# Performance work log

Hardware: AMD Instinct MI355X
Metric: run time of the kernel (lower is better)

## Reference

```python
import jax, jax.numpy as jnp
import numpy as np

K = 7          # kernel_size
PAD = 3        # padding
GROUPS = 8
OUTC = 128
INC = 128
REFINE = True


def conv1x1(x, w):
    # x: [B,C,H,W], w: [O,C] (1x1 conv, no bias)
    return jnp.einsum('oc,bchw->bohw', w, x)


def unfold2d(x, k):
    # x: [B,C,Hp,Wp] -> [B,C,h,w,k,k], stride 1 (matches torch unfold(2,k).unfold(3,k))
    B, C, Hp, Wp = x.shape
    h, w = Hp - k + 1, Wp - k + 1
    patches = jnp.stack([x[:, :, i:i + h, j:j + w] for i in range(k) for j in range(k)], axis=-1)
    return patches.reshape(B, C, h, w, k, k)


def unfold1d(x, k, axis):
    # sliding window of size k, stride 1, along axis 2 (rows) or 3 (cols)
    if axis == 2:
        h = x.shape[2] - k + 1
        return jnp.stack([x[:, :, i:i + h, :] for i in range(k)], axis=-1)  # [B,C,h,W,k]
    else:
        w = x.shape[3] - k + 1
        return jnp.stack([x[:, :, :, j:j + w] for j in range(k)], axis=-1)  # [B,C,H,w,k]


def _forward(feature_map, wq, wk, wv, rel_h, rel_w):
    c = feature_map.shape[1] // 2
    fm_t0, fm_t1 = feature_map[:, :c], feature_map[:, c:]
    B, _, H, W = fm_t0.shape
    cg = OUTC // GROUPS

    padded_t0 = jnp.pad(fm_t0, ((0, 0), (0, 0), (PAD, PAD), (PAD, PAD)))
    q = conv1x1(fm_t1, wq)                 # [B,OUTC,H,W]
    k_full = conv1x1(padded_t0, wk)        # [B,OUTC,H+2p,W+2p]
    v_full = conv1x1(padded_t0, wv)

    k_win = unfold2d(k_full, K)            # [B,OUTC,H,W,K,K]
    k_h, k_w = k_win[:, :OUTC // 2], k_win[:, OUTC // 2:]
    k_win = jnp.concatenate([k_h + rel_h, k_w + rel_w], axis=1)
    k_win = k_win.reshape(B, GROUPS, cg, H, W, K * K)
    v_win = unfold2d(v_full, K).reshape(B, GROUPS, cg, H, W, K * K)

    qg = q.reshape(B, GROUPS, cg, H, W, 1)
    attn = jax.nn.softmax(jnp.sum(qg * k_win, axis=2), axis=-1)  # [B,G,H,W,K*K]
    out = jnp.einsum('bnhwk,bnchwk->bnchw', attn, v_win).reshape(B, OUTC, H, W)

    if REFINE:
        win = 2 * K + 1
        p_col = jnp.pad(fm_t0, ((0, 0), (0, 0), (K, K), (0, 0)))
        p_row = jnp.pad(fm_t0, ((0, 0), (0, 0), (0, 0), (K, K)))
        k_col = unfold1d(conv1x1(p_col, wk), win, 2).reshape(B, GROUPS, cg, H, W, win)
        k_row = unfold1d(conv1x1(p_row, wk), win, 3).reshape(B, GROUPS, cg, H, W, win)
        v_col = unfold1d(conv1x1(p_col, wv), win, 2).reshape(B, GROUPS, cg, H, W, win)
        v_row = unfold1d(conv1x1(p_row, wv), win, 3).reshape(B, GROUPS, cg, H, W, win)

        a_row = jax.nn.softmax(jnp.sum(qg * k_row, axis=2), axis=-1)
        a_col = jax.nn.softmax(jnp.sum(qg * k_col, axis=2), axis=-1)
        out = out + jnp.einsum('bnhwk,bnchwk->bnchw', a_row, v_row).reshape(B, OUTC, H, W)
        out = out + jnp.einsum('bnhwk,bnchwk->bnchw', a_col, v_col).reshape(B, OUTC, H, W)
    return out


def setup_inputs() -> dict:
    key = jax.random.key(0)
    ks = jax.random.split(key, 6)
    B, H, W = 2, 64, 64
    feature_map = jax.random.normal(ks[0], (B, 2 * INC, H, W), dtype=jnp.float32)
    # kaiming_normal fan_out for 1x1 conv: std = sqrt(2 / outc)
    std = float(np.sqrt(2.0 / OUTC))
    wq = jax.random.normal(ks[1], (OUTC, INC), dtype=jnp.float32) * std
    wk = jax.random.normal(ks[2], (OUTC, INC), dtype=jnp.float32) * std
    wv = jax.random.normal(ks[3], (OUTC, INC), dtype=jnp.float32) * std
    rel_h = jax.random.normal(ks[4], (OUTC // 2, 1, 1, K, 1), dtype=jnp.float32)
    rel_w = jax.random.normal(ks[5], (OUTC // 2, 1, 1, 1, K), dtype=jnp.float32)
    return {"feature_map": feature_map, "wq": wq, "wk": wk, "wv": wv,
            "rel_h": rel_h, "rel_w": rel_w}


def reference(feature_map, wq, wk, wv, rel_h, rel_w):
    return _forward(feature_map, wq, wk, wv, rel_h, rel_w)
```

## Files before the change

kernel.cpp:

```cpp
#include <hip/hip_runtime.h>
#include <hip/hip_bf16.h>

__device__ __forceinline__ float bf2f(unsigned short u) {
    union { unsigned int i; float f; } v; v.i = ((unsigned int)u) << 16; return v.f;
}
__device__ __forceinline__ unsigned short f2bf(float f) {
    __hip_bfloat16 h = __float2bfloat16(f);
    return *reinterpret_cast<unsigned short*>(&h);
}


__global__ __launch_bounds__(256) void conv_kernel(
    const float* __restrict__ fm,
    const float* __restrict__ wq, const float* __restrict__ wk,
    const float* __restrict__ wv,
    float* __restrict__ Qout,
    unsigned short* __restrict__ K0,
    unsigned short* __restrict__ V0)
{
    const int sel = blockIdx.y;
    const float* W = (sel == 0) ? wq : ((sel == 1) ? wk : wv);
    const int c0 = (sel == 0) ? 128 : 0;

    __shared__ float w_s[64 * 132];
    __shared__ float x_s[64 * 68];

    const int tid = threadIdx.x;
    const int P0  = blockIdx.x * 64;
    const int b   = P0 >> 12;
    const int hw0 = P0 & 4095;

    float acc[8][4];
    #pragma unroll
    for (int i = 0; i < 8; ++i)
        #pragma unroll
        for (int j = 0; j < 4; ++j) acc[i][j] = 0.f;

    const int ocb = (tid >> 4) * 8;
    const int pxb = (tid & 15) * 4;

    for (int kh = 0; kh < 128; kh += 64) {
        {
            const int o    = tid >> 1;
            const int koff = (tid & 1) * 32;
            #pragma unroll
            for (int i = 0; i < 8; ++i) {
                float4 v = *(const float4*)(W + o * 128 + kh + koff + i * 4);
                w_s[(koff + i * 4 + 0) * 132 + o] = v.x;
                w_s[(koff + i * 4 + 1) * 132 + o] = v.y;
                w_s[(koff + i * 4 + 2) * 132 + o] = v.z;
                w_s[(koff + i * 4 + 3) * 132 + o] = v.w;
            }
        }
        {
            const int c  = tid >> 2;
            const int pc = (tid & 3) * 16;
            const float* src = fm + (((size_t)(b * 256 + c0 + kh + c)) << 12) + hw0 + pc;
            #pragma unroll
            for (int i = 0; i < 4; ++i)
                *(float4*)(&x_s[c * 68 + pc + i * 4]) = *(const float4*)(src + i * 4);
        }
        __syncthreads();
        #pragma unroll 8
        for (int k = 0; k < 64; ++k) {
            const float* kw = &w_s[k * 132 + ocb];
            float4 wa = *(const float4*)kw;
            float4 wb = *(const float4*)(kw + 4);
            float4 xv = *(const float4*)(&x_s[k * 68 + pxb]);
            const float wf[8] = {wa.x, wa.y, wa.z, wa.w, wb.x, wb.y, wb.z, wb.w};
            const float xf[4] = {xv.x, xv.y, xv.z, xv.w};
            #pragma unroll
            for (int i = 0; i < 8; ++i)
                #pragma unroll
                for (int j = 0; j < 4; ++j) acc[i][j] += wf[i] * xf[j];
        }
        __syncthreads();
    }

    const int g   = ocb >> 4;
    const int lci = ocb & 8;
    #pragma unroll
    for (int pj = 0; pj < 4; ++pj) {
        const int hw = hw0 + pxb + pj;
        const size_t base = ((((size_t)(b * 8 + g)) << 12) + hw) * 16 + lci;
        if (sel == 0) {
            *(float4*)(Qout + base)     = make_float4(acc[0][pj], acc[1][pj], acc[2][pj], acc[3][pj]);
            *(float4*)(Qout + base + 4) = make_float4(acc[4][pj], acc[5][pj], acc[6][pj], acc[7][pj]);
        } else {
            unsigned short tmp[8];
            #pragma unroll
            for (int i = 0; i < 8; ++i) tmp[i] = f2bf(acc[i][pj]);
            unsigned short* dst = ((sel == 1) ? K0 : V0) + base;
            *(uint4*)dst = *(const uint4*)tmp;
        }
    }
}

struct KV16 { uint4 a, b; };
__device__ __forceinline__ KV16 ld16(const unsigned short* p) {
    KV16 r; r.a = *(const uint4*)p; r.b = *(const uint4*)(p + 8); return r;
}
__device__ __forceinline__ float dotq(const float* q, const KV16& k) {
    const unsigned short* u = (const unsigned short*)&k;
    float s = 0.f;
    #pragma unroll
    for (int c = 0; c < 16; ++c) s += q[c] * bf2f(u[c]);
    return s;
}
__device__ __forceinline__ void axpyq(float* acc, float wgt, const KV16& v) {
    const unsigned short* u = (const unsigned short*)&v;
    #pragma unroll
    for (int c = 0; c < 16; ++c) acc[c] += wgt * bf2f(u[c]);
}

__global__ __launch_bounds__(256) void attn_kernel(
    const float* __restrict__ Q,
    const unsigned short* __restrict__ K0,
    const unsigned short* __restrict__ V0,
    const float* __restrict__ rel_h,
    const float* __restrict__ rel_w,
    float* __restrict__ out)
{
    const int tid  = threadIdx.x;
    const int w    = tid & 63;
    const int h    = blockIdx.x * 4 + (tid >> 6);
    const int g    = blockIdx.y;
    const int b    = blockIdx.z / 3;
    const int part = blockIdx.z % 3;

    const size_t slab = ((size_t)(b * 8 + g)) << 16;
    const float* qptr = Q + slab + (size_t)(h * 64 + w) * 16;

    float qr[16];
    #pragma unroll
    for (int ci = 0; ci < 16; ++ci) qr[ci] = qptr[ci];

    const unsigned short* Kp = K0 + slab;
    const unsigned short* Vp = V0 + slab;

    float acc[16];
    #pragma unroll
    for (int ci = 0; ci < 16; ++ci) acc[ci] = 0.f;

    if (part == 0) {
        float qrel[7];
        const float* rel = (g < 4) ? (rel_h + g * 112) : (rel_w + (g - 4) * 112);
        #pragma unroll
        for (int t = 0; t < 7; ++t) {
            float s = 0.f;
            #pragma unroll
            for (int ci = 0; ci < 16; ++ci) s += qr[ci] * rel[ci * 7 + t];
            qrel[t] = s;
        }
        float sc[49];
        float mx = -3.4e38f;
        #pragma unroll
        for (int i = 0; i < 7; ++i) {
            const int y = h + i - 3;
            #pragma unroll
            for (int j = 0; j < 7; ++j) {
                const int x = w + j - 3;
                float d = 0.f;
                if (y >= 0 && y < 64 && x >= 0 && x < 64)
                    d = dotq(qr, ld16(Kp + (size_t)(y * 64 + x) * 16));
                d += qrel[(g < 4) ? i : j];
                sc[i * 7 + j] = d;
                mx = fmaxf(mx, d);
            }
        }
        float den = 0.f;
        #pragma unroll
        for (int k = 0; k < 49; ++k) { sc[k] = __expf(sc[k] - mx); den += sc[k]; }
        const float inv = 1.f / den;
        #pragma unroll
        for (int i = 0; i < 7; ++i) {
            const int y = h + i - 3;
            #pragma unroll
            for (int j = 0; j < 7; ++j) {
                const int x = w + j - 3;
                if (y >= 0 && y < 64 && x >= 0 && x < 64)
                    axpyq(acc, sc[i * 7 + j] * inv, ld16(Vp + (size_t)(y * 64 + x) * 16));
            }
        }
    } else if (part == 1) {
        float sc[15];
        float mx = -3.4e38f;
        #pragma unroll
        for (int j = 0; j < 15; ++j) {
            const int x = w + j - 7;
            float d = 0.f;
            if (x >= 0 && x < 64)
                d = dotq(qr, ld16(Kp + (size_t)(h * 64 + x) * 16));
            sc[j] = d; mx = fmaxf(mx, d);
        }
        float den = 0.f;
        #pragma unroll
        for (int j = 0; j < 15; ++j) { sc[j] = __expf(sc[j] - mx); den += sc[j]; }
        const float inv = 1.f / den;
        #pragma unroll
        for (int j = 0; j < 15; ++j) {
            const int x = w + j - 7;
            if (x >= 0 && x < 64)
                axpyq(acc, sc[j] * inv, ld16(Vp + (size_t)(h * 64 + x) * 16));
        }
    } else {
        float sc[15];
        float mx = -3.4e38f;
        #pragma unroll
        for (int i = 0; i < 15; ++i) {
            const int y = h + i - 7;
            float d = 0.f;
            if (y >= 0 && y < 64)
                d = dotq(qr, ld16(Kp + (size_t)(y * 64 + w) * 16));
            sc[i] = d; mx = fmaxf(mx, d);
        }
        float den = 0.f;
        #pragma unroll
        for (int i = 0; i < 15; ++i) { sc[i] = __expf(sc[i] - mx); den += sc[i]; }
        const float inv = 1.f / den;
        #pragma unroll
        for (int i = 0; i < 15; ++i) {
            const int y = h + i - 7;
            if (y >= 0 && y < 64)
                axpyq(acc, sc[i] * inv, ld16(Vp + (size_t)(y * 64 + w) * 16));
        }
    }

    float* op = out + (((size_t)(b * 128 + g * 16)) << 12) + h * 64 + w;
    #pragma unroll
    for (int ci = 0; ci < 16; ++ci)
        atomicAdd(op + ((size_t)ci << 12), acc[ci]);
}

extern "C" void kernel_launch(void* const* d_in, const int* in_sizes, int n_in,
                              void* d_out, int out_size, void* d_ws, size_t ws_size,
                              hipStream_t stream) {
    (void)in_sizes; (void)n_in; (void)ws_size;
    const float* fm    = (const float*)d_in[0];
    const float* wq    = (const float*)d_in[1];
    const float* wk    = (const float*)d_in[2];
    const float* wv    = (const float*)d_in[3];
    const float* rel_h = (const float*)d_in[4];
    const float* rel_w = (const float*)d_in[5];

    float* Q = (float*)d_ws;
    unsigned short* K0 = (unsigned short*)(Q + 1048576);
    unsigned short* V0 = K0 + 1048576;

    hipMemsetAsync(d_out, 0, (size_t)out_size * sizeof(float), stream);
    conv_kernel<<<dim3(128, 3, 1), dim3(256), 0, stream>>>(
        fm, wq, wk, wv, Q, K0, V0);
    attn_kernel<<<dim3(16, 8, 6), dim3(256), 0, stream>>>(
        Q, K0, V0, rel_h, rel_w, (float*)d_out);
}
```

Measured before the change: 115.3 us.

## Split each pixel's 16 channels across four lanes with quad shuffle reductions

The attention kernel now gives each output pixel four threads, each owning four channels. Dot products are finished with xor-shuffle reductions across the quad, and the grid grows fourfold, with one block covering one image row. Key/value loads for a window row are also batched into registers before use. The aim is to cut per-thread register pressure (sc[49] plus 16-wide accumulators) and raise occupancy and memory parallelism. The cost is extra shuffles and redundant softmax work done by all four lanes.

```diff
diff --git a/kernel.cpp b/kernel.cpp
--- a/kernel.cpp
+++ b/kernel.cpp
@@ -96,21 +96,14 @@
     }
 }
 
-struct KV16 { uint4 a, b; };
-__device__ __forceinline__ KV16 ld16(const unsigned short* p) {
-    KV16 r; r.a = *(const uint4*)p; r.b = *(const uint4*)(p + 8); return r;
-}
-__device__ __forceinline__ float dotq(const float* q, const KV16& k) {
+__device__ __forceinline__ float quadsum(float v) {
+    v += __shfl_xor(v, 1);
+    v += __shfl_xor(v, 2);
+    return v;
+}
+__device__ __forceinline__ float dot4(const float4& q, uint2 k) {
     const unsigned short* u = (const unsigned short*)&k;
-    float s = 0.f;
-    #pragma unroll
-    for (int c = 0; c < 16; ++c) s += q[c] * bf2f(u[c]);
-    return s;
-}
-__device__ __forceinline__ void axpyq(float* acc, float wgt, const KV16& v) {
-    const unsigned short* u = (const unsigned short*)&v;
-    #pragma unroll
-    for (int c = 0; c < 16; ++c) acc[c] += wgt * bf2f(u[c]);
+    return q.x * bf2f(u[0]) + q.y * bf2f(u[1]) + q.z * bf2f(u[2]) + q.w * bf2f(u[3]);
 }
 
 __global__ __launch_bounds__(256) void attn_kernel(
@@ -122,48 +115,46 @@
     float* __restrict__ out)
 {
     const int tid  = threadIdx.x;
-    const int w    = tid & 63;
-    const int h    = blockIdx.x * 4 + (tid >> 6);
+    const int s    = tid & 3;
+    const int w    = tid >> 2;
+    const int h    = blockIdx.x;
     const int g    = blockIdx.y;
     const int b    = blockIdx.z / 3;
     const int part = blockIdx.z % 3;
 
     const size_t slab = ((size_t)(b * 8 + g)) << 16;
-    const float* qptr = Q + slab + (size_t)(h * 64 + w) * 16;
-
-    float qr[16];
-    #pragma unroll
-    for (int ci = 0; ci < 16; ++ci) qr[ci] = qptr[ci];
-
-    const unsigned short* Kp = K0 + slab;
-    const unsigned short* Vp = V0 + slab;
-
-    float acc[16];
-    #pragma unroll
-    for (int ci = 0; ci < 16; ++ci) acc[ci] = 0.f;
+    const float4 qv = *(const float4*)(Q + slab + (size_t)(h * 64 + w) * 16 + s * 4);
+    const unsigned short* Kb = K0 + slab + s * 4;
+    const unsigned short* Vb = V0 + slab + s * 4;
+
+    float a0 = 0.f, a1 = 0.f, a2 = 0.f, a3 = 0.f;
+    const uint2 z2 = make_uint2(0u, 0u);
 
     if (part == 0) {
         float qrel[7];
-        const float* rel = (g < 4) ? (rel_h + g * 112) : (rel_w + (g - 4) * 112);
+        const float* rel = (g < 4) ? (rel_h + (g * 16 + s * 4) * 7)
+                                   : (rel_w + ((g - 4) * 16 + s * 4) * 7);
         #pragma unroll
         for (int t = 0; t < 7; ++t) {
-            float s = 0.f;
-            #pragma unroll
-            for (int ci = 0; ci < 16; ++ci) s += qr[ci] * rel[ci * 7 + t];
-            qrel[t] = s;
+            float pq = qv.x * rel[t] + qv.y * rel[7 + t]
+                     + qv.z * rel[14 + t] + qv.w * rel[21 + t];
+            qrel[t] = quadsum(pq);
         }
         float sc[49];
         float mx = -3.4e38f;
         #pragma unroll
         for (int i = 0; i < 7; ++i) {
             const int y = h + i - 3;
+            uint2 kr[7];
             #pragma unroll
             for (int j = 0; j < 7; ++j) {
                 const int x = w + j - 3;
-                float d = 0.f;
-                if (y >= 0 && y < 64 && x >= 0 && x < 64)
-                    d = dotq(qr, ld16(Kp + (size_t)(y * 64 + x) * 16));
-                d += qrel[(g < 4) ? i : j];
+                kr[j] = (y >= 0 && y < 64 && x >= 0 && x < 64)
+                      ? *(const uint2*)(Kb + (size_t)(y * 64 + x) * 16) : z2;
+            }
+            #pragma unroll
+            for (int j = 0; j < 7; ++j) {
+                float d = quadsum(dot4(qv, kr[j])) + qrel[(g < 4) ? i : j];
                 sc[i * 7 + j] = d;
                 mx = fmaxf(mx, d);
             }
@@ -175,22 +166,33 @@
         #pragma unroll
         for (int i = 0; i < 7; ++i) {
             const int y = h + i - 3;
+            uint2 vr[7];
             #pragma unroll
             for (int j = 0; j < 7; ++j) {
                 const int x = w + j - 3;
-                if (y >= 0 && y < 64 && x >= 0 && x < 64)
-                    axpyq(acc, sc[i * 7 + j] * inv, ld16(Vp + (size_t)(y * 64 + x) * 16));
+                vr[j] = (y >= 0 && y < 64 && x >= 0 && x < 64)
+                      ? *(const uint2*)(Vb + (size_t)(y * 64 + x) * 16) : z2;
+            }
+            #pragma unroll
+            for (int j = 0; j < 7; ++j) {
+                const float pw = sc[i * 7 + j] * inv;
+                const unsigned short* u = (const unsigned short*)&vr[j];
+                a0 += pw * bf2f(u[0]); a1 += pw * bf2f(u[1]);
+                a2 += pw * bf2f(u[2]); a3 += pw * bf2f(u[3]);
             }
         }
     } else if (part == 1) {
         float sc[15];
         float mx = -3.4e38f;
+        uint2 kr[15];
         #pragma unroll
         for (int j = 0; j < 15; ++j) {
             const int x = w + j - 7;
-            float d = 0.f;
-            if (x >= 0 && x < 64)
-                d = dotq(qr, ld16(Kp + (size_t)(h * 64 + x) * 16));
+            kr[j] = (x >= 0 && x < 64) ? *(const uint2*)(Kb + (size_t)(h * 64 + x) * 16) : z2;
+        }
+        #pragma unroll
+        for (int j = 0; j < 15; ++j) {
+            float d = quadsum(dot4(qv, kr[j]));
             sc[j] = d; mx = fmaxf(mx, d);
         }
         float den = 0.f;
@@ -200,18 +202,24 @@
         #pragma unroll
         for (int j = 0; j < 15; ++j) {
             const int x = w + j - 7;
-            if (x >= 0 && x < 64)
-                axpyq(acc, sc[j] * inv, ld16(Vp + (size_t)(h * 64 + x) * 16));
+            uint2 vv = (x >= 0 && x < 64) ? *(const uint2*)(Vb + (size_t)(h * 64 + x) * 16) : z2;
+            const float pw = sc[j] * inv;
+            const unsigned short* u = (const unsigned short*)&vv;
+            a0 += pw * bf2f(u[0]); a1 += pw * bf2f(u[1]);
+            a2 += pw * bf2f(u[2]); a3 += pw * bf2f(u[3]);
         }
     } else {
         float sc[15];
         float mx = -3.4e38f;
+        uint2 kr[15];
         #pragma unroll
         for (int i = 0; i < 15; ++i) {
             const int y = h + i - 7;
-            float d = 0.f;
-            if (y >= 0 && y < 64)
-                d = dotq(qr, ld16(Kp + (size_t)(y * 64 + w) * 16));
+            kr[i] = (y >= 0 && y < 64) ? *(const uint2*)(Kb + (size_t)(y * 64 + w) * 16) : z2;
+        }
+        #pragma unroll
+        for (int i = 0; i < 15; ++i) {
+            float d = quadsum(dot4(qv, kr[i]));
             sc[i] = d; mx = fmaxf(mx, d);
         }
         float den = 0.f;
@@ -221,15 +229,19 @@
         #pragma unroll
         for (int i = 0; i < 15; ++i) {
             const int y = h + i - 7;
-            if (y >= 0 && y < 64)
-                axpyq(acc, sc[i] * inv, ld16(Vp + (size_t)(y * 64 + w) * 16));
+            uint2 vv = (y >= 0 && y < 64) ? *(const uint2*)(Vb + (size_t)(y * 64 + w) * 16) : z2;
+            const float pw = sc[i] * inv;
+            const unsigned short* u = (const unsigned short*)&vv;
+            a0 += pw * bf2f(u[0]); a1 += pw * bf2f(u[1]);
+            a2 += pw * bf2f(u[2]); a3 += pw * bf2f(u[3]);
         }
     }
 
-    float* op = out + (((size_t)(b * 128 + g * 16)) << 12) + h * 64 + w;
-    #pragma unroll
-    for (int ci = 0; ci < 16; ++ci)
-        atomicAdd(op + ((size_t)ci << 12), acc[ci]);
+    float* op = out + (((size_t)(b * 128 + g * 16 + s * 4)) << 12) + h * 64 + w;
+    atomicAdd(op,                       a0);
+    atomicAdd(op + ((size_t)1 << 12),   a1);
+    atomicAdd(op + ((size_t)2 << 12),   a2);
+    atomicAdd(op + ((size_t)3 << 12),   a3);
 }
 
 extern "C" void kernel_launch(void* const* d_in, const int* in_sizes, int n_in,
@@ -250,6 +262,6 @@
     hipMemsetAsync(d_out, 0, (size_t)out_size * sizeof(float), stream);
     conv_kernel<<<dim3(128, 3, 1), dim3(256), 0, stream>>>(
         fm, wq, wk, wv, Q, K0, V0);
-    attn_kernel<<<dim3(16, 8, 6), dim3(256), 0, stream>>>(
+    attn_kernel<<<dim3(64, 8, 6), dim3(256), 0, stream>>>(
         Q, K0, V0, rel_h, rel_w, (float*)d_out);
 }
```

Result: slower. 182.8 us (+58.6%).

## Stage K/V tiles in shared memory, split attention into row/col kernels, drop atomics

Applied to the files above, without the earlier changes.

The attention stage is split into two kernels. One handles the 7x7 window and the row window, working from a 10-row K/V tile staged in LDS, and writes the output directly. The other stages a transposed 4-column tile and adds the column-window result with a plain read-modify-write. This removes the memset, the global atomics and the repeated global K/V gathers. The conv kernel uses 32-pixel tiles to launch twice as many blocks. The cost is an extra launch, fewer blocks in the attention grid, and LDS use that may reduce occupancy.

```diff
diff --git a/kernel.cpp b/kernel.cpp
--- a/kernel.cpp
+++ b/kernel.cpp
@@ -23,21 +23,19 @@
     const int c0 = (sel == 0) ? 128 : 0;
 
     __shared__ float w_s[64 * 132];
-    __shared__ float x_s[64 * 68];
+    __shared__ float x_s[64 * 36];
 
     const int tid = threadIdx.x;
-    const int P0  = blockIdx.x * 64;
+    const int P0  = blockIdx.x * 32;
     const int b   = P0 >> 12;
     const int hw0 = P0 & 4095;
 
-    float acc[8][4];
-    #pragma unroll
-    for (int i = 0; i < 8; ++i)
-        #pragma unroll
-        for (int j = 0; j < 4; ++j) acc[i][j] = 0.f;
+    float acc[8][2];
+    #pragma unroll
+    for (int i = 0; i < 8; ++i) { acc[i][0] = 0.f; acc[i][1] = 0.f; }
 
     const int ocb = (tid >> 4) * 8;
-    const int pxb = (tid & 15) * 4;
+    const int pxb = (tid & 15) * 2;
 
     for (int kh = 0; kh < 128; kh += 64) {
         {
@@ -54,11 +52,10 @@
         }
         {
             const int c  = tid >> 2;
-            const int pc = (tid & 3) * 16;
+            const int pc = (tid & 3) * 8;
             const float* src = fm + (((size_t)(b * 256 + c0 + kh + c)) << 12) + hw0 + pc;
-            #pragma unroll
-            for (int i = 0; i < 4; ++i)
-                *(float4*)(&x_s[c * 68 + pc + i * 4]) = *(const float4*)(src + i * 4);
+            *(float4*)(&x_s[c * 36 + pc])     = *(const float4*)src;
+            *(float4*)(&x_s[c * 36 + pc + 4]) = *(const float4*)(src + 4);
         }
         __syncthreads();
         #pragma unroll 8
@@ -66,13 +63,13 @@
             const float* kw = &w_s[k * 132 + ocb];
             float4 wa = *(const float4*)kw;
             float4 wb = *(const float4*)(kw + 4);
-            float4 xv = *(const float4*)(&x_s[k * 68 + pxb]);
+            float2 xv = *(const float2*)(&x_s[k * 36 + pxb]);
             const float wf[8] = {wa.x, wa.y, wa.z, wa.w, wb.x, wb.y, wb.z, wb.w};
-            const float xf[4] = {xv.x, xv.y, xv.z, xv.w};
-            #pragma unroll
-            for (int i = 0; i < 8; ++i)
-                #pragma unroll
-                for (int j = 0; j < 4; ++j) acc[i][j] += wf[i] * xf[j];
+            #pragma unroll
+            for (int i = 0; i < 8; ++i) {
+                acc[i][0] += wf[i] * xv.x;
+                acc[i][1] += wf[i] * xv.y;
+            }
         }
         __syncthreads();
     }
@@ -80,7 +77,7 @@
     const int g   = ocb >> 4;
     const int lci = ocb & 8;
     #pragma unroll
-    for (int pj = 0; pj < 4; ++pj) {
+    for (int pj = 0; pj < 2; ++pj) {
         const int hw = hw0 + pxb + pj;
         const size_t base = ((((size_t)(b * 8 + g)) << 12) + hw) * 16 + lci;
         if (sel == 0) {
@@ -96,24 +93,7 @@
     }
 }
 
-struct KV16 { uint4 a, b; };
-__device__ __forceinline__ KV16 ld16(const unsigned short* p) {
-    KV16 r; r.a = *(const uint4*)p; r.b = *(const uint4*)(p + 8); return r;
-}
-__device__ __forceinline__ float dotq(const float* q, const KV16& k) {
-    const unsigned short* u = (const unsigned short*)&k;
-    float s = 0.f;
-    #pragma unroll
-    for (int c = 0; c < 16; ++c) s += q[c] * bf2f(u[c]);
-    return s;
-}
-__device__ __forceinline__ void axpyq(float* acc, float wgt, const KV16& v) {
-    const unsigned short* u = (const unsigned short*)&v;
-    #pragma unroll
-    for (int c = 0; c < 16; ++c) acc[c] += wgt * bf2f(u[c]);
-}
-
-__global__ __launch_bounds__(256) void attn_kernel(
+__global__ __launch_bounds__(256) void attnA_kernel(
     const float* __restrict__ Q,
     const unsigned short* __restrict__ K0,
     const unsigned short* __restrict__ V0,
@@ -121,29 +101,49 @@
     const float* __restrict__ rel_w,
     float* __restrict__ out)
 {
-    const int tid  = threadIdx.x;
-    const int w    = tid & 63;
-    const int h    = blockIdx.x * 4 + (tid >> 6);
-    const int g    = blockIdx.y;
-    const int b    = blockIdx.z / 3;
-    const int part = blockIdx.z % 3;
-
+    __shared__ __align__(16) unsigned short ks[10 * 64 * 16];
+    __shared__ __align__(16) unsigned short vs[10 * 64 * 16];
+
+    const int tid = threadIdx.x;
+    const int ty  = tid >> 6;
+    const int w   = tid & 63;
+    const int h0  = blockIdx.x * 4;
+    const int h   = h0 + ty;
+    const int g   = blockIdx.y;
+    const int b   = blockIdx.z;
     const size_t slab = ((size_t)(b * 8 + g)) << 16;
-    const float* qptr = Q + slab + (size_t)(h * 64 + w) * 16;
+
+    {
+        const uint4* Ksrc = (const uint4*)(K0 + slab);
+        const uint4* Vsrc = (const uint4*)(V0 + slab);
+        uint4* kd = (uint4*)ks;
+        uint4* vd = (uint4*)vs;
+        #pragma unroll
+        for (int it = 0; it < 5; ++it) {
+            const int idx = tid + it * 256;
+            const int row = idx >> 7;
+            const int off = idx & 127;
+            const int rg  = h0 - 3 + row;
+            uint4 kz = make_uint4(0u,0u,0u,0u), vz = make_uint4(0u,0u,0u,0u);
+            if (rg >= 0 && rg < 64) {
+                kz = Ksrc[rg * 128 + off];
+                vz = Vsrc[rg * 128 + off];
+            }
+            kd[idx] = kz;
+            vd[idx] = vz;
+        }
+    }
+    __syncthreads();
 
     float qr[16];
-    #pragma unroll
-    for (int ci = 0; ci < 16; ++ci) qr[ci] = qptr[ci];
-
-    const unsigned short* Kp = K0 + slab;
-    const unsigned short* Vp = V0 + slab;
-
-    float acc[16];
-    #pragma unroll
-    for (int ci = 0; ci < 16; ++ci) acc[ci] = 0.f;
-
-    if (part == 0) {
-        float qrel[7];
+    {
+        const float* qp = Q + slab + (size_t)(h * 64 + w) * 16;
+        #pragma unroll
+        for (int ci = 0; ci < 16; ++ci) qr[ci] = qp[ci];
+    }
+
+    float qrel[7];
+    {
         const float* rel = (g < 4) ? (rel_h + g * 112) : (rel_w + (g - 4) * 112);
         #pragma unroll
         for (int t = 0; t < 7; ++t) {
@@ -152,17 +152,28 @@
             for (int ci = 0; ci < 16; ++ci) s += qr[ci] * rel[ci * 7 + t];
             qrel[t] = s;
         }
+    }
+
+    float acc[16];
+    #pragma unroll
+    for (int ci = 0; ci < 16; ++ci) acc[ci] = 0.f;
+
+    {
         float sc[49];
         float mx = -3.4e38f;
         #pragma unroll
         for (int i = 0; i < 7; ++i) {
-            const int y = h + i - 3;
+            const unsigned short* krow = ks + (ty + i) * 64 * 16;
             #pragma unroll
             for (int j = 0; j < 7; ++j) {
                 const int x = w + j - 3;
+                const bool xin = (unsigned)x < 64u;
+                const int xc = xin ? x : 0;
+                const unsigned short* kp = krow + xc * 16;
                 float d = 0.f;
-                if (y >= 0 && y < 64 && x >= 0 && x < 64)
-                    d = dotq(qr, ld16(Kp + (size_t)(y * 64 + x) * 16));
+                #pragma unroll
+                for (int c = 0; c < 16; ++c) d += qr[c] * bf2f(kp[c]);
+                d = xin ? d : 0.f;
                 d += qrel[(g < 4) ? i : j];
                 sc[i * 7 + j] = d;
                 mx = fmaxf(mx, d);
@@ -174,24 +185,36 @@
         const float inv = 1.f / den;
         #pragma unroll
         for (int i = 0; i < 7; ++i) {
-            const int y = h + i - 3;
+            const unsigned short* vrow = vs + (ty + i) * 64 * 16;
             #pragma unroll
             for (int j = 0; j < 7; ++j) {
                 const int x = w + j - 3;
-                if (y >= 0 && y < 64 && x >= 0 && x < 64)
-                    axpyq(acc, sc[i * 7 + j] * inv, ld16(Vp + (size_t)(y * 64 + x) * 16));
-            }
-        }
-    } else if (part == 1) {
+                const bool xin = (unsigned)x < 64u;
+                const int xc = xin ? x : 0;
+                const float pw = xin ? sc[i * 7 + j] * inv : 0.f;
+                const unsigned short* vp = vrow + xc * 16;
+                #pragma unroll
+                for (int c = 0; c < 16; ++c) acc[c] += pw * bf2f(vp[c]);
+            }
+        }
+    }
+    {
+        const unsigned short* krow = ks + (ty + 3) * 64 * 16;
+        const unsigned short* vrow = vs + (ty + 3) * 64 * 16;
         float sc[15];
         float mx = -3.4e38f;
         #pragma unroll
         for (int j = 0; j < 15; ++j) {
             const int x = w + j - 7;
+            const bool xin = (unsigned)x < 64u;
+            const int xc = xin ? x : 0;
+            const unsigned short* kp = krow + xc * 16;
             float d = 0.f;
-            if (x >= 0 && x < 64)
-                d = dotq(qr, ld16(Kp + (size_t)(h * 64 + x) * 16));
-            sc[j] = d; mx = fmaxf(mx, d);
+            #pragma unroll
+            for (int c = 0; c < 16; ++c) d += qr[c] * bf2f(kp[c]);
+            d = xin ? d : 0.f;
+            sc[j] = d;
+            mx = fmaxf(mx, d);
         }
         float den = 0.f;
         #pragma unroll
@@ -200,42 +223,113 @@
         #pragma unroll
         for (int j = 0; j < 15; ++j) {
             const int x = w + j - 7;
-            if (x >= 0 && x < 64)
-                axpyq(acc, sc[j] * inv, ld16(Vp + (size_t)(h * 64 + x) * 16));
-        }
-    } else {
-        float sc[15];
-        float mx = -3.4e38f;
-        #pragma unroll
-        for (int i = 0; i < 15; ++i) {
-            const int y = h + i - 7;
-            float d = 0.f;
-            if (y >= 0 && y < 64)
-                d = dotq(qr, ld16(Kp + (size_t)(y * 64 + w) * 16));
-            sc[i] = d; mx = fmaxf(mx, d);
-        }
-        float den = 0.f;
-        #pragma unroll
-        for (int i = 0; i < 15; ++i) { sc[i] = __expf(sc[i] - mx); den += sc[i]; }
-        const float inv = 1.f / den;
-        #pragma unroll
-        for (int i = 0; i < 15; ++i) {
-            const int y = h + i - 7;
-            if (y >= 0 && y < 64)
-                axpyq(acc, sc[i] * inv, ld16(Vp + (size_t)(y * 64 + w) * 16));
+            const bool xin = (unsigned)x < 64u;
+            const int xc = xin ? x : 0;
+            const float pw = xin ? sc[j] * inv : 0.f;
+            const unsigned short* vp = vrow + xc * 16;
+            #pragma unroll
+            for (int c = 0; c < 16; ++c) acc[c] += pw * bf2f(vp[c]);
         }
     }
 
     float* op = out + (((size_t)(b * 128 + g * 16)) << 12) + h * 64 + w;
     #pragma unroll
-    for (int ci = 0; ci < 16; ++ci)
-        atomicAdd(op + ((size_t)ci << 12), acc[ci]);
+    for (int ci = 0; ci < 16; ++ci) op[(size_t)ci << 12] = acc[ci];
+}
+
+__global__ __launch_bounds__(256) void attnB_kernel(
+    const float* __restrict__ Q,
+    const unsigned short* __restrict__ K0,
+    const unsigned short* __restrict__ V0,
+    float* __restrict__ out)
+{
+    __shared__ __align__(16) unsigned short ks[4 * 64 * 16];
+    __shared__ __align__(16) unsigned short vs[4 * 64 * 16];
+
+    const int tid = threadIdx.x;
+    const int wl  = tid >> 6;
+    const int h   = tid & 63;
+    const int w0  = blockIdx.x * 4;
+    const int g   = blockIdx.y;
+    const int b   = blockIdx.z;
+    const size_t slab = ((size_t)(b * 8 + g)) << 16;
+
+    {
+        const uint4* Ksrc = (const uint4*)(K0 + slab);
+        const uint4* Vsrc = (const uint4*)(V0 + slab);
+        uint4* kd = (uint4*)ks;
+        uint4* vd = (uint4*)vs;
+        #pragma unroll
+        for (int it = 0; it < 2; ++it) {
+            const int idx  = tid + it * 256;
+            const int hh   = idx >> 3;
+            const int rem  = idx & 7;
+            const int wp   = rem >> 1;
+            const int half = rem & 1;
+            const int gidx = (hh * 64 + w0 + wp) * 2 + half;
+            const int lidx = (wp * 64 + hh) * 2 + half;
+            kd[lidx] = Ksrc[gidx];
+            vd[lidx] = Vsrc[gidx];
+        }
+    }
+    __syncthreads();
+
+    float qr[16];
+    {
+        const float* qp = Q + slab + (size_t)(h * 64 + w0 + wl) * 16;
+        #pragma unroll
+        for (int ci = 0; ci < 16; ++ci) qr[ci] = qp[ci];
+    }
+
+    const unsigned short* kcol = ks + wl * 64 * 16;
+    const unsigned short* vcol = vs + wl * 64 * 16;
+
+    float sc[15];
+    float mx = -3.4e38f;
+    #pragma unroll
+    for (int i = 0; i < 15; ++i) {
+        const int y = h + i - 7;
+        const bool yin = (unsigned)y < 64u;
+        const int yc = yin ? y : 0;
+        const unsigned short* kp = kcol + yc * 16;
+        float d = 0.f;
+        #pragma unroll
+        for (int c = 0; c < 16; ++c) d += qr[c] * bf2f(kp[c]);
+        d = yin ? d : 0.f;
+        sc[i] = d;
+        mx = fmaxf(mx, d);
+    }
+    float den = 0.f;
+    #pragma unroll
+    for (int i = 0; i < 15; ++i) { sc[i] = __expf(sc[i] - mx); den += sc[i]; }
+    const float inv = 1.f / den;
+
+    float acc[16];
+    #pragma unroll
+    for (int ci = 0; ci < 16; ++ci) acc[ci] = 0.f;
+    #pragma unroll
+    for (int i = 0; i < 15; ++i) {
+        const int y = h + i - 7;
+        const bool yin = (unsigned)y < 64u;
+        const int yc = yin ? y : 0;
+        const float pw = yin ? sc[i] * inv : 0.f;
+        const unsigned short* vp = vcol + yc * 16;
+        #pragma unroll
+        for (int c = 0; c < 16; ++c) acc[c] += pw * bf2f(vp[c]);
+    }
+
+    float* op = out + (((size_t)(b * 128 + g * 16)) << 12) + h * 64 + (w0 + wl);
+    #pragma unroll
+    for (int ci = 0; ci < 16; ++ci) {
+        float* p = op + ((size_t)ci << 12);
+        *p = *p + acc[ci];
+    }
 }
 
 extern "C" void kernel_launch(void* const* d_in, const int* in_sizes, int n_in,
                               void* d_out, int out_size, void* d_ws, size_t ws_size,
                               hipStream_t stream) {
-    (void)in_sizes; (void)n_in; (void)ws_size;
+    (void)in_sizes; (void)n_in; (void)out_size; (void)ws_size;
     const float* fm    = (const float*)d_in[0];
     const float* wq    = (const float*)d_in[1];
     const float* wk    = (const float*)d_in[2];
@@ -247,9 +341,10 @@
     unsigned short* K0 = (unsigned short*)(Q + 1048576);
     unsigned short* V0 = K0 + 1048576;
 
-    hipMemsetAsync(d_out, 0, (size_t)out_size * sizeof(float), stream);
-    conv_kernel<<<dim3(128, 3, 1), dim3(256), 0, stream>>>(
+    conv_kernel<<<dim3(256, 3, 1), dim3(256), 0, stream>>>(
         fm, wq, wk, wv, Q, K0, V0);
-    attn_kernel<<<dim3(16, 8, 6), dim3(256), 0, stream>>>(
+    attnA_kernel<<<dim3(16, 8, 2), dim3(256), 0, stream>>>(
         Q, K0, V0, rel_h, rel_w, (float*)d_out);
-}
+    attnB_kernel<<<dim3(16, 8, 2), dim3(256), 0, stream>>>(
+        Q, K0, V0, (float*)d_out);
+}
```

Result: slower. 140.1 us (+21.5%).
